# Kernel optimization log

Hardware: AMD Instinct MI355X
Metric: run time of the kernel (lower is better)

The kernel has to match this reference:

```python
import jax, jax.numpy as jnp
import numpy as np

B, S, D, H = 4, 2048, 1024, 16
HD = D // H  # head_dim = 64


def setup_inputs() -> dict:
    key = jax.random.key(0)
    ks = jax.random.split(key, 9)
    sc = 0.02
    return {
        "x": jax.random.normal(ks[0], (B, S, D), dtype=jnp.float32),
        "mask": jnp.zeros((B, S), dtype=bool),  # True = masked
        "Wq": jax.random.normal(ks[1], (D, D), dtype=jnp.float32) * sc,
        "bq": jnp.zeros((D,), dtype=jnp.float32),
        "Wk": jax.random.normal(ks[2], (D, D), dtype=jnp.float32) * sc,
        "bk": jnp.zeros((D,), dtype=jnp.float32),
        "Wv": jax.random.normal(ks[3], (D, D), dtype=jnp.float32) * sc,
        "bv": jnp.zeros((D,), dtype=jnp.float32),
        "Wo": jax.random.normal(ks[4], (D, D), dtype=jnp.float32) * sc,
        "bo": jnp.zeros((D,), dtype=jnp.float32),
    }


def reference(x, mask, Wq, bq, Wk, bk, Wv, bv, Wo, bo):
    b, s, _ = x.shape
    scale = HD ** -0.5
    # projections, split heads: (b, h, s, hd)
    def heads(t):
        return t.reshape(b, s, H, HD).transpose(0, 2, 1, 3)
    q = heads(x @ Wq + bq)
    k = heads(x @ Wk + bk)
    v = heads(x @ Wv + bv)
    # scores: (b, h, s, s)
    attn = jnp.einsum('bhqd,bhkd->bhqk', q, k) * scale
    attn = jnp.where(mask[:, None, None, :], -jnp.inf, attn)
    attn = jax.nn.softmax(attn, axis=-1)
    # dropout p=0.0 -> identity (eval parity)
    out = jnp.einsum('bhqk,bhkd->bhqd', attn, v)
    out = out.transpose(0, 2, 1, 3).reshape(b, s, D)
    return out @ Wo + bo
```

## Files before the change

kernel.cpp:

```cpp
#include <hip/hip_runtime.h>
#include <cstdint>


typedef __bf16 bf16x8 __attribute__((ext_vector_type(8)));
typedef __bf16 bf16x4v __attribute__((ext_vector_type(4)));
typedef float f32x4 __attribute__((ext_vector_type(4)));
typedef unsigned u32x2 __attribute__((ext_vector_type(2)));
typedef unsigned u32x4 __attribute__((ext_vector_type(4)));

#define DEV __device__ __forceinline__

#if __has_builtin(__builtin_amdgcn_exp2f)
#define EXP2(x) __builtin_amdgcn_exp2f(x)
#else
#define EXP2(x) exp2f(x)
#endif

DEV __bf16 f2bf(float f) { return (__bf16)f; }

DEV void gload16(const void* g, void* l) {
  __builtin_amdgcn_global_load_lds(
      (const __attribute__((address_space(1))) unsigned int*)(uintptr_t)g,
      (__attribute__((address_space(3))) unsigned int*)(uintptr_t)l,
      16, 0, 0);
}

#define MFMA16(a, b, c) __builtin_amdgcn_mfma_f32_16x16x32_bf16((a), (b), (c), 0, 0, 0)

__global__ __launch_bounds__(256) void f2bf_vec4(const float4* __restrict__ in,
                                                 bf16x4v* __restrict__ out, int n4) {
  int i = blockIdx.x * blockDim.x + threadIdx.x;
  int stride = gridDim.x * blockDim.x;
  for (; i < n4; i += stride) {
    float4 v = in[i];
    bf16x4v o = { f2bf(v.x), f2bf(v.y), f2bf(v.z), f2bf(v.w) };
    out[i] = o;
  }
}

__global__ __launch_bounds__(256) void pack_mask(const unsigned char* __restrict__ mask,
                                                 unsigned* __restrict__ pm) {
  int t = threadIdx.x;
  int b = t >> 6, tile = (t >> 1) & 31, half = t & 1;
  unsigned bits = 0;
  for (int j = 0; j < 32; ++j)
    if (mask[b * 2048 + tile * 64 + half * 32 + j]) bits |= (1u << j);
  pm[b * 64 + tile * 2 + half] = bits;
}

__global__ __launch_bounds__(256) void pack_bias(const float* __restrict__ bq,
                                                 const float* __restrict__ bk,
                                                 const float* __restrict__ bv,
                                                 float* __restrict__ pb, float qs) {
  int i = blockIdx.x * 256 + threadIdx.x;
  float v = (i < 1024) ? bq[i] * qs : (i < 2048) ? bk[i - 1024] : bv[i - 2048];
  pb[i] = v;
}

__global__ __launch_bounds__(256) void transpose_w4(const float* __restrict__ w0,
                                                    const float* __restrict__ w1,
                                                    const float* __restrict__ w2,
                                                    const float* __restrict__ w3,
                                                    __bf16* __restrict__ dstb, float qs) {
  __shared__ float tile[32][33];
  const int which = blockIdx.z;
  const float* src = which == 0 ? w0 : which == 1 ? w1 : which == 2 ? w2 : w3;
  const float scale = (which == 0) ? qs : 1.0f;
  __bf16* dst = dstb + (size_t)which * 1024 * 1024;
  const int tx = threadIdx.x & 31;
  const int ty = threadIdx.x >> 5;
  const int x0 = blockIdx.x * 32;
  const int y0 = blockIdx.y * 32;
#pragma unroll
  for (int j = 0; j < 4; ++j)
    tile[ty + j * 8][tx] = src[(size_t)(y0 + ty + j * 8) * 1024 + x0 + tx];
  __syncthreads();
#pragma unroll
  for (int j = 0; j < 4; ++j)
    dst[(size_t)(x0 + ty + j * 8) * 1024 + y0 + tx] = f2bf(tile[tx][ty + j * 8] * scale);
}

__global__ __launch_bounds__(256, 4) void gemm128(const __bf16* __restrict__ A,
                                                  const __bf16* __restrict__ Bt,
                                                  const float* __restrict__ bias,
                                                  void* __restrict__ o0, void* __restrict__ o1,
                                                  void* __restrict__ o2, int mode) {
  constexpr int K = 1024;
  __shared__ alignas(16) __bf16 S[16384];
  __bf16* As_ = S;
  __bf16* Bs_ = S + 8192;
  const int t = threadIdx.x;
  const int lane = t & 63, w = t >> 6;
  const int g = lane >> 4, c = lane & 15;
  const int sw = c & 7;
  const int wm = w & 1, wn = w >> 1;
  const int bid = blockIdx.x;
  const int j = bid >> 3;
  const int m0 = (((bid & 7) << 3) + (j & 7)) << 7;
  const int n0 = (j >> 3) << 7;

  float bb4[4];
#pragma unroll
  for (int jj = 0; jj < 4; ++jj) bb4[jj] = bias[n0 + wn * 64 + jj * 16 + c];

  f32x4 acc[4][4];
#pragma unroll
  for (int i = 0; i < 4; ++i)
#pragma unroll
    for (int jj = 0; jj < 4; ++jj) acc[i][jj] = f32x4{0.f, 0.f, 0.f, 0.f};

#pragma unroll 1
  for (int kt = 0; kt < 16; ++kt) {
    const int k0 = kt << 6;
#pragma unroll
    for (int i = 0; i < 4; ++i) {
      int slot = i * 256 + t;
      int row = slot >> 3;
      int gch = (slot & 7) ^ (row & 7);
      gload16(&A[(size_t)(m0 + row) * K + k0 + gch * 8], &As_[slot * 8]);
      gload16(&Bt[(size_t)(n0 + row) * K + k0 + gch * 8], &Bs_[slot * 8]);
    }
    __syncthreads();
#pragma unroll
    for (int kk = 0; kk < 2; ++kk) {
      bf16x8 af[4], bfr[4];
#pragma unroll
      for (int i = 0; i < 4; ++i) {
        af[i]  = *(const bf16x8*)&As_[(wm * 64 + i * 16 + c) * 64 + (((kk * 4 + g) ^ sw) << 3)];
        bfr[i] = *(const bf16x8*)&Bs_[(wn * 64 + i * 16 + c) * 64 + (((kk * 4 + g) ^ sw) << 3)];
      }
#pragma unroll
      for (int i = 0; i < 4; ++i)
#pragma unroll
        for (int jj = 0; jj < 4; ++jj)
          acc[i][jj] = MFMA16(af[i], bfr[jj], acc[i][jj]);
    }
    __syncthreads();
  }

  const int bidx = m0 >> 11;
  const int s0g = m0 & 2047;

  if (mode == 2) {
#pragma unroll
    for (int i = 0; i < 4; ++i) {
      const int rowb = m0 + wm * 64 + i * 16 + g * 4;
#pragma unroll
      for (int jj = 0; jj < 4; ++jj) {
        const int col = n0 + wn * 64 + jj * 16 + c;
#pragma unroll
        for (int r = 0; r < 4; ++r)
          ((float*)o0)[(size_t)(rowb + r) * 1024 + col] = acc[i][jj][r] + bb4[jj];
      }
    }
    return;
  }

  const int seg = n0 >> 10;
  const int hb = (n0 & 1023) >> 6;
  unsigned short* LB = (unsigned short*)S;

#pragma unroll
  for (int hh = 0; hh < 2; ++hh) {
    __syncthreads();
    if (wn == hh) {
#pragma unroll
      for (int i = 0; i < 4; ++i) {
        const int rl = wm * 64 + i * 16 + g * 4;
#pragma unroll
        for (int jj = 0; jj < 4; ++jj) {
          const int col = jj * 16 + c;
#pragma unroll
          for (int r = 0; r < 4; ++r) {
            const int row = rl + r;
            __bf16 v = f2bf(acc[i][jj][r] + bb4[jj]);
            if (seg < 2) {
              LB[row * 72 + col] = __builtin_bit_cast(unsigned short, v);
            } else {
              int spl = (row & ~0x1C) | ((row & 0x0C) << 1) | ((row & 0x10) >> 2);
              LB[col * 136 + spl] = __builtin_bit_cast(unsigned short, v);
            }
          }
        }
      }
    }
    __syncthreads();
    if (seg < 2) {
      __bf16* dst = (__bf16*)(seg == 0 ? o0 : o1);
      const size_t hbase = ((size_t)(bidx * 16 + hb + hh) * 2048 + s0g) * 64;
#pragma unroll
      for (int s4 = 0; s4 < 4; ++s4) {
        int row = s4 * 32 + (t >> 3);
        int hd0 = (t & 7) * 8;
        bf16x8 v = *(const bf16x8*)&LB[row * 72 + hd0];
        *(bf16x8*)&dst[hbase + (size_t)row * 64 + hd0] = v;
      }
    } else {
      __bf16* dst = (__bf16*)o2;
      const int hd = t >> 2, q4 = t & 3;
      const size_t vb = ((size_t)(bidx * 16 + hb + hh) * 64 + hd) * 2048 + s0g;
#pragma unroll
      for (int kk = 0; kk < 4; ++kk) {
        int spb = q4 * 32 + kk * 8;
        bf16x8 v = *(const bf16x8*)&LB[hd * 136 + spb];
        *(bf16x8*)&dst[vb + spb] = v;
      }
    }
  }
}

__global__ __launch_bounds__(256, 4) void attn_kernel(const __bf16* __restrict__ q,
                                                      const __bf16* __restrict__ k,
                                                      const __bf16* __restrict__ vt,
                                                      const unsigned* __restrict__ pm,
                                                      __bf16* __restrict__ outp) {
  const int bid = blockIdx.x;
  const int xcd = bid & 7, j = bid >> 3;
  const int bh = xcd * 8 + (j & 7), qb = j >> 3;
  const int b = bh >> 4, h = bh & 15;
  const int t = threadIdx.x, lane = t & 63, w = t >> 6;
  const int g = lane >> 4, c = lane & 15;
  const int sw = c & 7;

  __shared__ alignas(16) __bf16 S[12288];
  __bf16* Vs = S + 8192;

  const size_t kbase = (size_t)bh * (2048 * 64);
  const size_t vbase = (size_t)bh * (64 * 2048);
  const int q0 = qb * 128 + w * 32;

  unsigned mword = pm[b * 64 + lane];

  bf16x8 qf[2][2];
#pragma unroll
  for (int i = 0; i < 2; ++i)
#pragma unroll
    for (int m = 0; m < 2; ++m)
      qf[i][m] = *(const bf16x8*)&q[kbase + (size_t)(q0 + i * 16 + c) * 64 + m * 32 + g * 8];
  asm volatile("" :: "v"(qf[0][0]), "v"(qf[0][1]), "v"(qf[1][0]), "v"(qf[1][1]),
                     "v"(mword) : "memory");

  f32x4 acc[2][4];
  f32x4 lacc[2];
#pragma unroll
  for (int i = 0; i < 2; ++i) {
    lacc[i] = f32x4{0.f, 0.f, 0.f, 0.f};
#pragma unroll
    for (int n = 0; n < 4; ++n) acc[i][n] = f32x4{0.f, 0.f, 0.f, 0.f};
  }

  const bf16x8 ones = { (__bf16)1.f, (__bf16)1.f, (__bf16)1.f, (__bf16)1.f,
                        (__bf16)1.f, (__bf16)1.f, (__bf16)1.f, (__bf16)1.f };

  auto stageK = [&](int bb, int kv0) {
#pragma unroll
    for (int r2 = 0; r2 < 2; ++r2) {
      int slot = r2 * 256 + t;
      int row = slot >> 3, ch = slot & 7;
      int gch = ch ^ (row & 7);
      gload16(&k[kbase + (size_t)(kv0 + row) * 64 + gch * 8], &S[bb * 4096 + slot * 8]);
    }
  };
  auto stageV = [&](int kv0) {
#pragma unroll
    for (int r2 = 0; r2 < 2; ++r2) {
      int slot = r2 * 256 + t;
      int row = slot >> 3, ch = slot & 7;
      int gch = ch ^ (row & 7);
      gload16(&vt[vbase + (size_t)row * 2048 + kv0 + gch * 8], &Vs[slot * 8]);
    }
  };

  stageK(0, 0);
  stageV(0);

#pragma unroll 1
  for (int kv = 0; kv < 32; ++kv) {
    const int bb = kv & 1;
    const int kv0 = kv << 6;
    if (kv < 31) {
      stageK(bb ^ 1, kv0 + 64);
      asm volatile("s_waitcnt vmcnt(2)" ::: "memory");
    } else {
      asm volatile("s_waitcnt vmcnt(0)" ::: "memory");
    }
    __builtin_amdgcn_s_barrier();

    const __bf16* ksb = S + (bb << 12);
    unsigned mwlo = __builtin_amdgcn_readlane(mword, 2 * kv);
    unsigned mwhi = __builtin_amdgcn_readlane(mword, 2 * kv + 1);

    __builtin_amdgcn_s_setprio(1);
    f32x4 sc[2][4];
#pragma unroll
    for (int n = 0; n < 4; ++n) {
      bf16x8 kf0 = *(const bf16x8*)&ksb[(n * 16 + c) * 64 + (((0 + g) ^ sw) << 3)];
      bf16x8 kf1 = *(const bf16x8*)&ksb[(n * 16 + c) * 64 + (((4 + g) ^ sw) << 3)];
#pragma unroll
      for (int i = 0; i < 2; ++i) {
        f32x4 z = f32x4{0.f, 0.f, 0.f, 0.f};
        z = MFMA16(kf0, qf[i][0], z);
        z = MFMA16(kf1, qf[i][1], z);
        sc[i][n] = z;
      }
    }
    __builtin_amdgcn_sched_barrier(0);

    u32x4 pf0[2];
    if (mwlo) {
#pragma unroll
      for (int n = 0; n < 2; ++n)
#pragma unroll
        for (int r = 0; r < 4; ++r)
          if ((mwlo >> (n * 16 + g * 4 + r)) & 1u) { sc[0][n][r] = -1e30f; sc[1][n][r] = -1e30f; }
    }
#pragma unroll
    for (int i = 0; i < 2; ++i) {
      float p0 = EXP2(sc[i][0][0]), p1 = EXP2(sc[i][0][1]);
      float p2 = EXP2(sc[i][0][2]), p3 = EXP2(sc[i][0][3]);
      float p4 = EXP2(sc[i][1][0]), p5 = EXP2(sc[i][1][1]);
      float p6 = EXP2(sc[i][1][2]), p7 = EXP2(sc[i][1][3]);
      unsigned w0, w1, w2, w3;
      asm("v_cvt_pk_bf16_f32 %0, %1, %2" : "=v"(w0) : "v"(p0), "v"(p1));
      asm("v_cvt_pk_bf16_f32 %0, %1, %2" : "=v"(w1) : "v"(p2), "v"(p3));
      asm("v_cvt_pk_bf16_f32 %0, %1, %2" : "=v"(w2) : "v"(p4), "v"(p5));
      asm("v_cvt_pk_bf16_f32 %0, %1, %2" : "=v"(w3) : "v"(p6), "v"(p7));
      pf0[i] = u32x4{w0, w1, w2, w3};
    }

#pragma unroll
    for (int n = 0; n < 4; ++n) {
      bf16x8 vf0 = *(const bf16x8*)&Vs[(n * 16 + c) * 64 + (((0 + g) ^ sw) << 3)];
#pragma unroll
      for (int i = 0; i < 2; ++i)
        acc[i][n] = MFMA16(vf0, __builtin_bit_cast(bf16x8, pf0[i]), acc[i][n]);
    }
#pragma unroll
    for (int i = 0; i < 2; ++i)
      lacc[i] = MFMA16(ones, __builtin_bit_cast(bf16x8, pf0[i]), lacc[i]);
    __builtin_amdgcn_sched_barrier(0);

    u32x4 pf1[2];
    if (mwhi) {
#pragma unroll
      for (int n = 2; n < 4; ++n)
#pragma unroll
        for (int r = 0; r < 4; ++r)
          if ((mwhi >> ((n - 2) * 16 + g * 4 + r)) & 1u) { sc[0][n][r] = -1e30f; sc[1][n][r] = -1e30f; }
    }
#pragma unroll
    for (int i = 0; i < 2; ++i) {
      float p0 = EXP2(sc[i][2][0]), p1 = EXP2(sc[i][2][1]);
      float p2 = EXP2(sc[i][2][2]), p3 = EXP2(sc[i][2][3]);
      float p4 = EXP2(sc[i][3][0]), p5 = EXP2(sc[i][3][1]);
      float p6 = EXP2(sc[i][3][2]), p7 = EXP2(sc[i][3][3]);
      unsigned w0, w1, w2, w3;
      asm("v_cvt_pk_bf16_f32 %0, %1, %2" : "=v"(w0) : "v"(p0), "v"(p1));
      asm("v_cvt_pk_bf16_f32 %0, %1, %2" : "=v"(w1) : "v"(p2), "v"(p3));
      asm("v_cvt_pk_bf16_f32 %0, %1, %2" : "=v"(w2) : "v"(p4), "v"(p5));
      asm("v_cvt_pk_bf16_f32 %0, %1, %2" : "=v"(w3) : "v"(p6), "v"(p7));
      pf1[i] = u32x4{w0, w1, w2, w3};
    }

#pragma unroll
    for (int n = 0; n < 4; ++n) {
      bf16x8 vf1 = *(const bf16x8*)&Vs[(n * 16 + c) * 64 + (((4 + g) ^ sw) << 3)];
#pragma unroll
      for (int i = 0; i < 2; ++i)
        acc[i][n] = MFMA16(vf1, __builtin_bit_cast(bf16x8, pf1[i]), acc[i][n]);
    }
#pragma unroll
    for (int i = 0; i < 2; ++i)
      lacc[i] = MFMA16(ones, __builtin_bit_cast(bf16x8, pf1[i]), lacc[i]);
    __builtin_amdgcn_s_setprio(0);

    __builtin_amdgcn_s_barrier();
    if (kv < 31) stageV(kv0 + 64);
  }

  float linv[2];
#pragma unroll
  for (int i = 0; i < 2; ++i) linv[i] = 1.0f / fmaxf(lacc[i][0], 1e-30f);

  __bf16* ot = S + w * 2176;
#pragma unroll
  for (int i = 0; i < 2; ++i)
#pragma unroll
    for (int n = 0; n < 4; ++n) {
      float a0 = acc[i][n][0] * linv[i], a1 = acc[i][n][1] * linv[i];
      float a2 = acc[i][n][2] * linv[i], a3 = acc[i][n][3] * linv[i];
      unsigned w0, w1;
      asm("v_cvt_pk_bf16_f32 %0, %1, %2" : "=v"(w0) : "v"(a0), "v"(a1));
      asm("v_cvt_pk_bf16_f32 %0, %1, %2" : "=v"(w1) : "v"(a2), "v"(a3));
      *(u32x2*)&ot[(i * 16 + c) * 68 + n * 16 + g * 4] = u32x2{w0, w1};
    }
  asm volatile("s_waitcnt lgkmcnt(0)" ::: "memory");
  __builtin_amdgcn_sched_barrier(0);
#pragma unroll
  for (int ps = 0; ps < 4; ++ps) {
    int rr = ps * 8 + (lane >> 3);
    bf16x8 ov = *(const bf16x8*)&ot[rr * 68 + (lane & 7) * 8];
    *(bf16x8*)&outp[((size_t)b * 2048 + q0 + rr) * 1024 + h * 64 + (lane & 7) * 8] = ov;
  }
}

extern "C" void kernel_launch(void* const* d_in, const int* in_sizes, int n_in,
                              void* d_out, int out_size, void* d_ws, size_t ws_size,
                              hipStream_t stream) {
  (void)in_sizes; (void)n_in; (void)out_size; (void)ws_size;
  const float* x  = (const float*)d_in[0];
  const unsigned char* mask = (const unsigned char*)d_in[1];
  const float* Wq = (const float*)d_in[2];
  const float* bq = (const float*)d_in[3];
  const float* Wk = (const float*)d_in[4];
  const float* bk = (const float*)d_in[5];
  const float* Wv = (const float*)d_in[6];
  const float* bv = (const float*)d_in[7];
  const float* Wo = (const float*)d_in[8];
  const float* bo = (const float*)d_in[9];
  float* out = (float*)d_out;

  char* ws = (char*)d_ws;
  const size_t SZ = (size_t)8192 * 1024 * 2;
  const size_t WSZ = (size_t)1024 * 1024 * 2;
  __bf16* xb  = (__bf16*)(ws);
  __bf16* qb  = (__bf16*)(ws + SZ);
  __bf16* kb  = (__bf16*)(ws + 2 * SZ);
  __bf16* vtb = (__bf16*)(ws + 3 * SZ);
  __bf16* wtq = (__bf16*)(ws + 4 * SZ);
  __bf16* wto = (__bf16*)(ws + 4 * SZ + 3 * WSZ);
  unsigned* pmask = (unsigned*)(ws + 4 * SZ + 4 * WSZ);
  float* pb = (float*)(ws + 4 * SZ + 4 * WSZ + 4096);

  const float QSCALE = 0.125f * 1.44269504f;

  f2bf_vec4<<<2048, 256, 0, stream>>>((const float4*)x, (bf16x4v*)xb, 8192 * 1024 / 4);
  pack_mask<<<1, 256, 0, stream>>>(mask, pmask);
  pack_bias<<<12, 256, 0, stream>>>(bq, bk, bv, pb, QSCALE);
  transpose_w4<<<dim3(32, 32, 4), 256, 0, stream>>>(Wq, Wk, Wv, Wo, wtq, QSCALE);
  gemm128<<<dim3(1536), 256, 0, stream>>>(xb, wtq, pb, qb, kb, vtb, 3);
  attn_kernel<<<dim3(1024), 256, 0, stream>>>(qb, kb, vtb, pmask, xb);
  gemm128<<<dim3(512), 256, 0, stream>>>(xb, wto, bo, out, nullptr, nullptr, 2);
}
```

Baseline: 173.8 us.

## Merge prep kernels; load V fragments directly from global with triple-buffered K

```diff
diff --git a/kernel.cpp b/kernel.cpp
--- a/kernel.cpp
+++ b/kernel.cpp
@@ -27,57 +27,55 @@
 
 #define MFMA16(a, b, c) __builtin_amdgcn_mfma_f32_16x16x32_bf16((a), (b), (c), 0, 0, 0)
 
-__global__ __launch_bounds__(256) void f2bf_vec4(const float4* __restrict__ in,
-                                                 bf16x4v* __restrict__ out, int n4) {
-  int i = blockIdx.x * blockDim.x + threadIdx.x;
-  int stride = gridDim.x * blockDim.x;
-  for (; i < n4; i += stride) {
-    float4 v = in[i];
-    bf16x4v o = { f2bf(v.x), f2bf(v.y), f2bf(v.z), f2bf(v.w) };
-    out[i] = o;
-  }
-}
-
-__global__ __launch_bounds__(256) void pack_mask(const unsigned char* __restrict__ mask,
-                                                 unsigned* __restrict__ pm) {
-  int t = threadIdx.x;
-  int b = t >> 6, tile = (t >> 1) & 31, half = t & 1;
-  unsigned bits = 0;
-  for (int j = 0; j < 32; ++j)
-    if (mask[b * 2048 + tile * 64 + half * 32 + j]) bits |= (1u << j);
-  pm[b * 64 + tile * 2 + half] = bits;
-}
-
-__global__ __launch_bounds__(256) void pack_bias(const float* __restrict__ bq,
-                                                 const float* __restrict__ bk,
-                                                 const float* __restrict__ bv,
-                                                 float* __restrict__ pb, float qs) {
-  int i = blockIdx.x * 256 + threadIdx.x;
-  float v = (i < 1024) ? bq[i] * qs : (i < 2048) ? bk[i - 1024] : bv[i - 2048];
-  pb[i] = v;
-}
-
-__global__ __launch_bounds__(256) void transpose_w4(const float* __restrict__ w0,
-                                                    const float* __restrict__ w1,
-                                                    const float* __restrict__ w2,
-                                                    const float* __restrict__ w3,
-                                                    __bf16* __restrict__ dstb, float qs) {
-  __shared__ float tile[32][33];
-  const int which = blockIdx.z;
-  const float* src = which == 0 ? w0 : which == 1 ? w1 : which == 2 ? w2 : w3;
-  const float scale = (which == 0) ? qs : 1.0f;
-  __bf16* dst = dstb + (size_t)which * 1024 * 1024;
-  const int tx = threadIdx.x & 31;
-  const int ty = threadIdx.x >> 5;
-  const int x0 = blockIdx.x * 32;
-  const int y0 = blockIdx.y * 32;
-#pragma unroll
-  for (int j = 0; j < 4; ++j)
-    tile[ty + j * 8][tx] = src[(size_t)(y0 + ty + j * 8) * 1024 + x0 + tx];
-  __syncthreads();
-#pragma unroll
-  for (int j = 0; j < 4; ++j)
-    dst[(size_t)(x0 + ty + j * 8) * 1024 + y0 + tx] = f2bf(tile[tx][ty + j * 8] * scale);
+__global__ __launch_bounds__(256) void prep(const float* __restrict__ x,
+                                            bf16x4v* __restrict__ xb,
+                                            const float* __restrict__ Wq,
+                                            const float* __restrict__ Wk,
+                                            const float* __restrict__ Wv,
+                                            const float* __restrict__ Wo,
+                                            __bf16* __restrict__ wtall, float qs,
+                                            const unsigned char* __restrict__ mask,
+                                            unsigned* __restrict__ pm,
+                                            const float* __restrict__ bq,
+                                            const float* __restrict__ bk,
+                                            const float* __restrict__ bv,
+                                            float* __restrict__ pb) {
+  const int blk = blockIdx.x, t = threadIdx.x;
+  if (blk < 2048) {
+    const float4* in = (const float4*)x;
+    int i = blk * 256 + t;
+    for (; i < 2097152; i += 2048 * 256) {
+      float4 v = in[i];
+      bf16x4v o = { f2bf(v.x), f2bf(v.y), f2bf(v.z), f2bf(v.w) };
+      xb[i] = o;
+    }
+  } else if (blk < 6144) {
+    __shared__ float tile[32][33];
+    const int idx = blk - 2048;
+    const int which = idx >> 10, tb = idx & 1023;
+    const float* src = which == 0 ? Wq : which == 1 ? Wk : which == 2 ? Wv : Wo;
+    const float scale = (which == 0) ? qs : 1.0f;
+    __bf16* dst = wtall + (size_t)which * 1024 * 1024;
+    const int tx = t & 31, ty = t >> 5;
+    const int x0 = (tb & 31) * 32, y0 = (tb >> 5) * 32;
+#pragma unroll
+    for (int j = 0; j < 4; ++j)
+      tile[ty + j * 8][tx] = src[(size_t)(y0 + ty + j * 8) * 1024 + x0 + tx];
+    __syncthreads();
+#pragma unroll
+    for (int j = 0; j < 4; ++j)
+      dst[(size_t)(x0 + ty + j * 8) * 1024 + y0 + tx] = f2bf(tile[tx][ty + j * 8] * scale);
+  } else {
+    int b = t >> 6, tl = (t >> 1) & 31, half = t & 1;
+    unsigned bits = 0;
+    for (int j = 0; j < 32; ++j)
+      if (mask[b * 2048 + tl * 64 + half * 32 + j]) bits |= (1u << j);
+    pm[b * 64 + tl * 2 + half] = bits;
+    for (int i = t; i < 3072; i += 256) {
+      float v = (i < 1024) ? bq[i] * qs : (i < 2048) ? bk[i - 1024] : bv[i - 2048];
+      pb[i] = v;
+    }
+  }
 }
 
 __global__ __launch_bounds__(256, 4) void gemm128(const __bf16* __restrict__ A,
@@ -223,7 +221,6 @@
   const int sw = c & 7;
 
   __shared__ alignas(16) __bf16 S[12288];
-  __bf16* Vs = S + 8192;
 
   const size_t kbase = (size_t)bh * (2048 * 64);
   const size_t vbase = (size_t)bh * (64 * 2048);
@@ -252,41 +249,36 @@
   const bf16x8 ones = { (__bf16)1.f, (__bf16)1.f, (__bf16)1.f, (__bf16)1.f,
                         (__bf16)1.f, (__bf16)1.f, (__bf16)1.f, (__bf16)1.f };
 
-  auto stageK = [&](int bb, int kv0) {
+  auto stageK = [&](int buf, int kv0) {
 #pragma unroll
     for (int r2 = 0; r2 < 2; ++r2) {
       int slot = r2 * 256 + t;
       int row = slot >> 3, ch = slot & 7;
       int gch = ch ^ (row & 7);
-      gload16(&k[kbase + (size_t)(kv0 + row) * 64 + gch * 8], &S[bb * 4096 + slot * 8]);
+      gload16(&k[kbase + (size_t)(kv0 + row) * 64 + gch * 8], &S[buf * 4096 + slot * 8]);
     }
   };
-  auto stageV = [&](int kv0) {
-#pragma unroll
-    for (int r2 = 0; r2 < 2; ++r2) {
-      int slot = r2 * 256 + t;
-      int row = slot >> 3, ch = slot & 7;
-      int gch = ch ^ (row & 7);
-      gload16(&vt[vbase + (size_t)row * 2048 + kv0 + gch * 8], &Vs[slot * 8]);
-    }
-  };
 
   stageK(0, 0);
-  stageV(0);
 
 #pragma unroll 1
   for (int kv = 0; kv < 32; ++kv) {
-    const int bb = kv & 1;
     const int kv0 = kv << 6;
+    const __bf16* ksb = S + (kv % 3) * 4096;
+    const __bf16* vrow = &vt[vbase + kv0];
+
+    if (kv < 31) stageK((kv + 1) % 3, kv0 + 64);
+    bf16x8 vf0[4];
+#pragma unroll
+    for (int n = 0; n < 4; ++n)
+      vf0[n] = *(const bf16x8*)&vrow[(size_t)(n * 16 + c) * 2048 + g * 8];
     if (kv < 31) {
-      stageK(bb ^ 1, kv0 + 64);
-      asm volatile("s_waitcnt vmcnt(2)" ::: "memory");
+      asm volatile("s_waitcnt vmcnt(6)" ::: "memory");
     } else {
-      asm volatile("s_waitcnt vmcnt(0)" ::: "memory");
+      asm volatile("s_waitcnt vmcnt(4)" ::: "memory");
     }
     __builtin_amdgcn_s_barrier();
 
-    const __bf16* ksb = S + (bb << 12);
     unsigned mwlo = __builtin_amdgcn_readlane(mword, 2 * kv);
     unsigned mwhi = __builtin_amdgcn_readlane(mword, 2 * kv + 1);
 
@@ -329,15 +321,19 @@
     }
 
 #pragma unroll
-    for (int n = 0; n < 4; ++n) {
-      bf16x8 vf0 = *(const bf16x8*)&Vs[(n * 16 + c) * 64 + (((0 + g) ^ sw) << 3)];
+    for (int n = 0; n < 4; ++n)
 #pragma unroll
       for (int i = 0; i < 2; ++i)
-        acc[i][n] = MFMA16(vf0, __builtin_bit_cast(bf16x8, pf0[i]), acc[i][n]);
-    }
+        acc[i][n] = MFMA16(vf0[n], __builtin_bit_cast(bf16x8, pf0[i]), acc[i][n]);
 #pragma unroll
     for (int i = 0; i < 2; ++i)
       lacc[i] = MFMA16(ones, __builtin_bit_cast(bf16x8, pf0[i]), lacc[i]);
+    __builtin_amdgcn_sched_barrier(0);
+
+    bf16x8 vf1[4];
+#pragma unroll
+    for (int n = 0; n < 4; ++n)
+      vf1[n] = *(const bf16x8*)&vrow[(size_t)(n * 16 + c) * 2048 + (4 + g) * 8];
     __builtin_amdgcn_sched_barrier(0);
 
     u32x4 pf1[2];
@@ -363,20 +359,17 @@
     }
 
 #pragma unroll
-    for (int n = 0; n < 4; ++n) {
-      bf16x8 vf1 = *(const bf16x8*)&Vs[(n * 16 + c) * 64 + (((4 + g) ^ sw) << 3)];
+    for (int n = 0; n < 4; ++n)
 #pragma unroll
       for (int i = 0; i < 2; ++i)
-        acc[i][n] = MFMA16(vf1, __builtin_bit_cast(bf16x8, pf1[i]), acc[i][n]);
-    }
+        acc[i][n] = MFMA16(vf1[n], __builtin_bit_cast(bf16x8, pf1[i]), acc[i][n]);
 #pragma unroll
     for (int i = 0; i < 2; ++i)
       lacc[i] = MFMA16(ones, __builtin_bit_cast(bf16x8, pf1[i]), lacc[i]);
     __builtin_amdgcn_s_setprio(0);
-
-    __builtin_amdgcn_s_barrier();
-    if (kv < 31) stageV(kv0 + 64);
-  }
+  }
+
+  __syncthreads();
 
   float linv[2];
 #pragma unroll
@@ -434,10 +427,8 @@
 
   const float QSCALE = 0.125f * 1.44269504f;
 
-  f2bf_vec4<<<2048, 256, 0, stream>>>((const float4*)x, (bf16x4v*)xb, 8192 * 1024 / 4);
-  pack_mask<<<1, 256, 0, stream>>>(mask, pmask);
-  pack_bias<<<12, 256, 0, stream>>>(bq, bk, bv, pb, QSCALE);
-  transpose_w4<<<dim3(32, 32, 4), 256, 0, stream>>>(Wq, Wk, Wv, Wo, wtq, QSCALE);
+  prep<<<dim3(6145), 256, 0, stream>>>(x, (bf16x4v*)xb, Wq, Wk, Wv, Wo, wtq, QSCALE,
+                                       mask, pmask, bq, bk, bv, pb);
   gemm128<<<dim3(1536), 256, 0, stream>>>(xb, wtq, pb, qb, kb, vtb, 3);
   attn_kernel<<<dim3(1024), 256, 0, stream>>>(qb, kb, vtb, pmask, xb);
   gemm128<<<dim3(512), 256, 0, stream>>>(xb, wto, bo, out, nullptr, nullptr, 2);
```

After: 243.6 us. +40.1%, slower.
